# Performance work log

Measured on AMD Instinct MI355X. Metric: run time of the kernel, lower is better.

The kernel has to match this reference:

```python
import jax, jax.numpy as jnp
import numpy as np

B, S, D, H = 2, 2048, 1024, 16
DH = D // H


def setup_inputs() -> dict:
    key = jax.random.key(0)
    ks = jax.random.split(key, 12)
    std = 1.0 / np.sqrt(D)
    inp = {
        "q": jax.random.normal(ks[0], (B, S, D), jnp.float32),
        "k": jax.random.normal(ks[1], (B, S, D), jnp.float32),
        "v": jax.random.normal(ks[2], (B, S, D), jnp.float32),
        "mask": jnp.tril(jnp.ones((S, S), jnp.bool_))[None, None],  # causal [1,1,S,S]
        "wq_w": jax.random.uniform(ks[3], (D, D), jnp.float32, -std, std),
        "wq_b": jax.random.uniform(ks[4], (D,), jnp.float32, -std, std),
        "wk_w": jax.random.uniform(ks[5], (D, D), jnp.float32, -std, std),
        "wk_b": jax.random.uniform(ks[6], (D,), jnp.float32, -std, std),
        "wv_w": jax.random.uniform(ks[7], (D, D), jnp.float32, -std, std),
        "wv_b": jax.random.uniform(ks[8], (D,), jnp.float32, -std, std),
        "wo_w": jax.random.uniform(ks[9], (D, D), jnp.float32, -std, std),
        "wo_b": jax.random.uniform(ks[10], (D,), jnp.float32, -std, std),
    }
    return inp


def reference(q, k, v, mask, wq_w, wq_b, wk_w, wk_b, wv_w, wv_b, wo_w, wo_b):
    b, s, d = q.shape
    dh = d // H
    scale = jnp.sqrt(jnp.asarray(dh, q.dtype))  # scale = d_model/n_heads = d_head

    def proj(x, w, bias):
        y = x @ w.T + bias
        return y.reshape(b, -1, H, dh).transpose(0, 2, 1, 3)  # [B,H,S,dh]

    Q = proj(q, wq_w, wq_b)
    K = proj(k, wk_w, wk_b)
    V = proj(v, wv_w, wv_b)

    score = jnp.einsum("bhqd,bhkd->bhqk", Q, K) / scale
    score = jnp.where(mask, score, jnp.asarray(-1e10, score.dtype))
    attn = jax.nn.softmax(score, axis=-1)
    # dropout is identity in eval mode
    y = jnp.einsum("bhqk,bhkd->bhqd", attn, V)
    y = y.transpose(0, 2, 1, 3).reshape(b, -1, d)
    y = y @ wo_w.T + wo_b
    return y, attn
```

## Files before the change

kernel.cpp:

```cpp
#include <hip/hip_runtime.h>
#include <cstdint>

#define S_LEN   2048
#define D_MODEL 1024
#define NHEAD   16
#define DHEAD   64
#define BATCH   2
#define M_ROWS  (BATCH * S_LEN)

typedef __attribute__((ext_vector_type(8))) short bf16x8;
typedef __attribute__((ext_vector_type(4))) float f32x4;

__device__ __forceinline__ unsigned short f2bf(float f) {
    union { float f; uint32_t u; } v; v.f = f;
    uint32_t u = v.u;
    return (unsigned short)((u + 0x7FFFu + ((u >> 16) & 1u)) >> 16);
}

__device__ __forceinline__ float bf2f(uint32_t u16) {
    union { uint32_t u; float f; } x; x.u = u16 << 16; return x.f;
}

__device__ __forceinline__ uint32_t cvt_pk_bf16(float a, float b) {
    uint32_t r;
    asm("v_cvt_pk_bf16_f32 %0, %1, %2" : "=v"(r) : "v"(a), "v"(b));
    return r;
}

__device__ __forceinline__ void gload_lds16(const void* g, void* l) {
    __builtin_amdgcn_global_load_lds(
        (const __attribute__((address_space(1))) void*)g,
        (__attribute__((address_space(3))) void*)l, 16, 0, 0);
}

struct CvtArgs {
    const float* src[7];
    unsigned short* dst[7];
    int n4[7];
};
__global__ __launch_bounds__(256) void cvt_all(CvtArgs a) {
    const int which = blockIdx.y;
    const int t = blockIdx.x * 256 + threadIdx.x;
    if (t >= a.n4[which]) return;
    f32x4 v = reinterpret_cast<const f32x4*>(a.src[which])[t];
    uint2 o;
    o.x = cvt_pk_bf16(v[0], v[1]);
    o.y = cvt_pk_bf16(v[2], v[3]);
    reinterpret_cast<uint2*>(a.dst[which])[t] = o;
}

template<int MODE>
__device__ __forceinline__ void gemm_body(
    unsigned short* lA, unsigned short* lB,
    const unsigned short* __restrict__ A,
    const unsigned short* __restrict__ Bw,
    const float* __restrict__ bias,
    void* __restrict__ Cout,
    int bx, int by, float prescale)
{
    constexpr int K = 1024;
    const int tid  = threadIdx.x;
    const int lane = tid & 63;
    const int w    = tid >> 6;
    const int wr   = w >> 1, wc = w & 1;
    const int g    = lane >> 4, r16 = lane & 15;
    const int brow = by * 128;
    const int bcol = bx * 128;

    f32x4 acc[4][4];
#pragma unroll
    for (int i = 0; i < 4; ++i)
#pragma unroll
        for (int j = 0; j < 4; ++j) acc[i][j] = (f32x4){0.f, 0.f, 0.f, 0.f};

    const int rA0 = tid >> 2;
    const int cc  = (tid & 3) * 8;

    for (int kk = 0; kk < K; kk += 32) {
#pragma unroll
        for (int it = 0; it < 2; ++it) {
            int r = it * 64 + rA0;
            gload_lds16(A  + (size_t)(brow + r) * K + kk + cc, &lA[r * 32 + cc]);
            gload_lds16(Bw + (size_t)(bcol + r) * K + kk + cc, &lB[r * 32 + cc]);
        }
        __syncthreads();
        bf16x8 af[4], bfr[4];
#pragma unroll
        for (int i = 0; i < 4; ++i)
            af[i] = *reinterpret_cast<const bf16x8*>(&lA[(wr * 64 + i * 16 + r16) * 32 + g * 8]);
#pragma unroll
        for (int j = 0; j < 4; ++j)
            bfr[j] = *reinterpret_cast<const bf16x8*>(&lB[(wc * 64 + j * 16 + r16) * 32 + g * 8]);
#pragma unroll
        for (int i = 0; i < 4; ++i)
#pragma unroll
            for (int j = 0; j < 4; ++j)
                acc[i][j] = __builtin_amdgcn_mfma_f32_16x16x32_bf16(af[i], bfr[j], acc[i][j], 0, 0, 0);
        __syncthreads();
    }

#pragma unroll
    for (int i = 0; i < 4; ++i) {
#pragma unroll
        for (int j = 0; j < 4; ++j) {
            const int n = bcol + wc * 64 + j * 16 + r16;
#pragma unroll
            for (int rr = 0; rr < 4; ++rr) {
                const int m = brow + wr * 64 + i * 16 + g * 4 + rr;
                float val = acc[i][j][rr];
                if (MODE == 0) {
                    val = (val + bias[n]) * prescale;
                    int b = m >> 11, s = m & 2047;
                    int h = n >> 6,  d = n & 63;
                    ((unsigned short*)Cout)[(((size_t)(b * NHEAD + h)) * S_LEN + s) * DHEAD + d] = f2bf(val);
                } else if (MODE == 1) {
                    val += bias[m];
                    int h = m >> 6,  d = m & 63;
                    int b = n >> 11, s = n & 2047;
                    ((unsigned short*)Cout)[(((size_t)(b * NHEAD + h)) * DHEAD + d) * S_LEN + s] = f2bf(val);
                } else {
                    val += bias[n];
                    ((float*)Cout)[(size_t)m * D_MODEL + n] = val;
                }
            }
        }
    }
}

__global__ __launch_bounds__(256) void proj_all(
    const unsigned short* qb, const unsigned short* wqb, const float* wq_b, unsigned short* Qhp,
    const unsigned short* kb, const unsigned short* wkb, const float* wk_b, unsigned short* Khp,
    const unsigned short* vb, const unsigned short* wvb, const float* wv_b, unsigned short* Vtp,
    float qscale)
{
    __shared__ unsigned short lA[128 * 32];
    __shared__ unsigned short lB[128 * 32];
    const int bid = blockIdx.x;
    const int z = bid >> 8, t = bid & 255;
    if (z == 0)
        gemm_body<0>(lA, lB, qb, wqb, wq_b, Qhp, t & 7, t >> 3, qscale);
    else if (z == 1)
        gemm_body<0>(lA, lB, kb, wkb, wk_b, Khp, t & 7, t >> 3, 1.0f);
    else
        gemm_body<1>(lA, lB, wvb, vb, wv_b, Vtp, t & 31, t >> 5, 1.0f);
}

__global__ __launch_bounds__(512, 2) void attn_ctx_kernel(
    const unsigned short* __restrict__ Qh,
    const unsigned short* __restrict__ Kh,
    const unsigned short* __restrict__ Vt,
    float* __restrict__ stats,
    unsigned short* __restrict__ ctx)
{
    __shared__ unsigned short ldsK[2][64 * 64];
    __shared__ unsigned short ldsV[2][64 * 64];
    __shared__ unsigned short pS[8][16 * 72];

    const int tid  = threadIdx.x;
    const int lane = tid & 63;
    const int w    = tid >> 6;
    const int g    = lane >> 4, r16 = lane & 15;
    const int wg   = w & 3;
    const int grp  = w >> 2;

    const int lid = blockIdx.x;
    const int xcd = lid & 7;
    const int rest = lid >> 3;
    const int bh  = xcd * 4 + (rest >> 3);
    const int ii  = rest & 7;
    const int b   = bh >> 4, h = bh & 15;

    const unsigned short* Kp = Kh + (size_t)bh * S_LEN * DHEAD;
    const unsigned short* Vp = Vt + (size_t)bh * DHEAD * S_LEN;

    const int srow = tid >> 3;
    const int scol = (tid & 7) * 16;
    const int sswz = scol ^ ((srow & 7) << 4);
    const int rsw  = (r16 & 7) << 4;

    unsigned short* pl = pS[w];

    for (int pp = 0; pp < 2; ++pp) {
        const int p  = pp == 0 ? ii : 15 - ii;
        const int qh = 16 + p;
        const int ql = 15 - p;
        const int qtile = grp == 0 ? qh : ql;
        const int qw    = qtile * 64 + wg * 16;
        const int qrel  = wg * 16 + r16;
        const int myN   = qtile;

        const unsigned short* Qp = Qh + ((size_t)bh * S_LEN + qw) * DHEAD;
        bf16x8 qf[2];
#pragma unroll
        for (int d2 = 0; d2 < 2; ++d2)
            qf[d2] = *reinterpret_cast<const bf16x8*>(Qp + (size_t)r16 * DHEAD + d2 * 32 + g * 8);

        auto stageKV = [&](int kt, int buf) {
            gload_lds16((const char*)Kp + (size_t)(kt * 64 + srow) * 128 + sswz,
                        (char*)ldsK[buf] + tid * 16);
            gload_lds16((const char*)Vp + (size_t)srow * (S_LEN * 2) + (size_t)kt * 128 + sswz,
                        (char*)ldsV[buf] + tid * 16);
        };

        float l_run = 0.f;
        f32x4 of[4];
#pragma unroll
        for (int nt = 0; nt < 4; ++nt) of[nt] = (f32x4){0, 0, 0, 0};

        int buf = 0;
        stageKV(0, 0);
        __syncthreads();
        for (int t = 0; t <= qh; ++t) {
            if (t < qh) stageKV(t + 1, buf ^ 1);
            if (t <= myN) {
                const bool masked = (t == myN);
                bf16x8 kf[8];
#pragma unroll
                for (int d2 = 0; d2 < 2; ++d2)
#pragma unroll
                    for (int nt = 0; nt < 4; ++nt)
                        kf[d2 * 4 + nt] = *reinterpret_cast<const bf16x8*>(
                            (const char*)ldsK[buf] + (nt * 16 + r16) * 128 + ((d2 * 64 + g * 16) ^ rsw));
                f32x4 sf[4];
#pragma unroll
                for (int nt = 0; nt < 4; ++nt) sf[nt] = (f32x4){0, 0, 0, 0};
                __builtin_amdgcn_s_setprio(1);
#pragma unroll
                for (int d2 = 0; d2 < 2; ++d2)
#pragma unroll
                    for (int nt = 0; nt < 4; ++nt)
                        sf[nt] = __builtin_amdgcn_mfma_f32_16x16x32_bf16(kf[d2 * 4 + nt], qf[d2], sf[nt], 0, 0, 0);
                __builtin_amdgcn_s_setprio(0);
                float sum = 0.f;
#pragma unroll
                for (int nt = 0; nt < 4; ++nt)
#pragma unroll
                    for (int rr = 0; rr < 4; ++rr) {
                        float e = __builtin_amdgcn_exp2f(sf[nt][rr]);
                        if (masked && (nt * 16 + g * 4 + rr > qrel)) e = 0.f;
                        sf[nt][rr] = e;
                        sum += e;
                    }
                l_run += sum;
#pragma unroll
                for (int nt = 0; nt < 4; ++nt) {
                    uint2 pk2;
                    pk2.x = cvt_pk_bf16(sf[nt][0], sf[nt][1]);
                    pk2.y = cvt_pk_bf16(sf[nt][2], sf[nt][3]);
                    *reinterpret_cast<uint2*>(&pl[r16 * 72 + nt * 16 + g * 4]) = pk2;
                }
                __builtin_amdgcn_wave_barrier();
                __builtin_amdgcn_s_setprio(1);
#pragma unroll
                for (int kh = 0; kh < 2; ++kh) {
                    bf16x8 pa = *reinterpret_cast<const bf16x8*>(&pl[r16 * 72 + kh * 32 + g * 8]);
#pragma unroll
                    for (int nt = 0; nt < 4; ++nt) {
                        bf16x8 vf = *reinterpret_cast<const bf16x8*>(
                            (const char*)ldsV[buf] + (nt * 16 + r16) * 128 + ((kh * 64 + g * 16) ^ rsw));
                        of[nt] = __builtin_amdgcn_mfma_f32_16x16x32_bf16(vf, pa, of[nt], 0, 0, 0);
                    }
                }
                __builtin_amdgcn_s_setprio(0);
            }
            __syncthreads();
            buf ^= 1;
        }

        float lx = l_run;
        lx += __shfl_xor(lx, 16);
        lx += __shfl_xor(lx, 32);
        const float mprime = __builtin_amdgcn_logf(lx);
        if (lane < 16)
            stats[(size_t)bh * S_LEN + qw + r16] = mprime;

        const float inv = 1.f / lx;
        const size_t crow = ((size_t)b * S_LEN + qw + r16) * D_MODEL + h * DHEAD;
#pragma unroll
        for (int nt = 0; nt < 4; ++nt) {
            uint2 pk2;
            pk2.x = cvt_pk_bf16(of[nt][0] * inv, of[nt][1] * inv);
            pk2.y = cvt_pk_bf16(of[nt][2] * inv, of[nt][3] * inv);
            *reinterpret_cast<uint2*>(&ctx[crow + nt * 16 + g * 4]) = pk2;
        }
        __syncthreads();
    }
}

__global__ __launch_bounds__(256) void fused_out(
    const unsigned short* __restrict__ ctx,
    const unsigned short* __restrict__ wob,
    const float* __restrict__ wo_b,
    float* __restrict__ yout,
    const unsigned short* __restrict__ Qh,
    const unsigned short* __restrict__ Kh,
    const float* __restrict__ stats,
    float* __restrict__ attn_out)
{
    __shared__ unsigned short lds[64 * 136 + 64];
    const int bid = blockIdx.x;
    if (bid < 256) {
        gemm_body<2>(lds, lds + 128 * 32, ctx, wob, wo_b, yout, bid & 7, bid >> 3, 1.0f);
        return;
    }

    const int tid  = threadIdx.x;
    const int lane = tid & 63;
    const int w    = tid >> 6;
    const int g    = lane >> 4, r16 = lane & 15;
    const int rl   = lane >> 4;
    const int c4   = (lane & 15) * 4;

    const int pid = bid - 256;
    const int xcd = pid & 7;
    const int cid = pid >> 3;
    const int bh  = xcd * 4 + cid / 272;
    const int t   = cid % 272;
    int m = (int)((sqrtf(4.f * t + 1.f) - 1.f) * 0.5f);
    while (m * (m + 1) > t) --m;
    while ((m + 1) * (m + 2) <= t) ++m;
    int qt, c2;
    if (t < (m + 1) * (m + 1)) { qt = 2 * m;     c2 = t - m * (m + 1); }
    else                       { qt = 2 * m + 1; c2 = t - (m + 1) * (m + 1); }

    float* abase = attn_out + (size_t)bh * S_LEN * S_LEN;

    const f32x4 z4 = (f32x4){0.f, 0.f, 0.f, 0.f};
#pragma unroll
    for (int s = 0; s < 2; ++s) {
        const int tr = 2 * c2 + s;
        if (qt > tr) {
            float* dstZ = abase + (size_t)(tr * 64) * S_LEN + qt * 64;
#pragma unroll
            for (int i = 0; i < 4; ++i) {
                const int r = w * 16 + i * 4 + rl;
                __builtin_nontemporal_store(z4,
                    reinterpret_cast<f32x4*>(dstZ + (size_t)r * S_LEN + c4));
            }
        }
    }

    const int qw   = qt * 64 + w * 16;
    const int qrel = w * 16 + r16;
    const unsigned short* Qp = Qh + ((size_t)bh * S_LEN + qw) * DHEAD;
    const unsigned short* Kp = Kh + (size_t)bh * S_LEN * DHEAD;

    bf16x8 qf[2];
#pragma unroll
    for (int d2 = 0; d2 < 2; ++d2)
        qf[d2] = *reinterpret_cast<const bf16x8*>(Qp + (size_t)r16 * DHEAD + d2 * 32 + g * 8);
    const float mpr = stats[(size_t)bh * S_LEN + qw + r16];

    unsigned short* plw = lds + w * (16 * 136);

#pragma unroll
    for (int kl = 0; kl < 2; ++kl) {
        const int kt = 2 * c2 + kl;
        if (kt > qt) {
            const uint2 zz = {0u, 0u};
#pragma unroll
            for (int nt = 0; nt < 4; ++nt)
                *reinterpret_cast<uint2*>(&plw[r16 * 136 + kl * 64 + nt * 16 + g * 4]) = zz;
            continue;
        }
        bf16x8 kf[8];
#pragma unroll
        for (int d2 = 0; d2 < 2; ++d2)
#pragma unroll
            for (int nt = 0; nt < 4; ++nt)
                kf[d2 * 4 + nt] = *reinterpret_cast<const bf16x8*>(
                    Kp + (size_t)(kt * 64 + nt * 16 + r16) * DHEAD + d2 * 32 + g * 8);
        f32x4 sf[4];
#pragma unroll
        for (int nt = 0; nt < 4; ++nt) sf[nt] = (f32x4){0, 0, 0, 0};
        __builtin_amdgcn_s_setprio(1);
#pragma unroll
        for (int d2 = 0; d2 < 2; ++d2)
#pragma unroll
            for (int nt = 0; nt < 4; ++nt)
                sf[nt] = __builtin_amdgcn_mfma_f32_16x16x32_bf16(kf[d2 * 4 + nt], qf[d2], sf[nt], 0, 0, 0);
        __builtin_amdgcn_s_setprio(0);
        const bool masked = (kt == qt);
#pragma unroll
        for (int nt = 0; nt < 4; ++nt) {
#pragma unroll
            for (int rr = 0; rr < 4; ++rr) {
                float p = __builtin_amdgcn_exp2f(sf[nt][rr] - mpr);
                if (masked && (nt * 16 + g * 4 + rr > qrel)) p = 0.f;
                sf[nt][rr] = p;
            }
            uint2 pk2;
            pk2.x = cvt_pk_bf16(sf[nt][0], sf[nt][1]);
            pk2.y = cvt_pk_bf16(sf[nt][2], sf[nt][3]);
            *reinterpret_cast<uint2*>(&plw[r16 * 136 + kl * 64 + nt * 16 + g * 4]) = pk2;
        }
    }
    __builtin_amdgcn_wave_barrier();

    float* dst0 = abase + (size_t)qw * S_LEN + c2 * 128;
    const int rsub = lane >> 5;
    const int cc2  = (lane & 31) * 4;
#pragma unroll
    for (int i = 0; i < 8; ++i) {
        const int r = i * 2 + rsub;
        uint2 d = *reinterpret_cast<const uint2*>(&plw[r * 136 + cc2]);
        f32x4 o;
        o[0] = bf2f(d.x & 0xffffu);
        o[1] = bf2f(d.x >> 16);
        o[2] = bf2f(d.y & 0xffffu);
        o[3] = bf2f(d.y >> 16);
        __builtin_nontemporal_store(o, reinterpret_cast<f32x4*>(dst0 + (size_t)r * S_LEN + cc2));
    }
}

extern "C" void kernel_launch(void* const* d_in, const int* in_sizes, int n_in,
                              void* d_out, int out_size, void* d_ws, size_t ws_size,
                              hipStream_t stream)
{
    const float* q    = (const float*)d_in[0];
    const float* k    = (const float*)d_in[1];
    const float* v    = (const float*)d_in[2];
    const float* wq_w = (const float*)d_in[4];
    const float* wq_b = (const float*)d_in[5];
    const float* wk_w = (const float*)d_in[6];
    const float* wk_b = (const float*)d_in[7];
    const float* wv_w = (const float*)d_in[8];
    const float* wv_b = (const float*)d_in[9];
    const float* wo_w = (const float*)d_in[10];
    const float* wo_b = (const float*)d_in[11];

    char* ws = (char*)d_ws;
    const size_t MB = 1024 * 1024;
    unsigned short* qb  = (unsigned short*)(ws + 0 * MB);
    unsigned short* kb  = (unsigned short*)(ws + 8 * MB);
    unsigned short* vb  = (unsigned short*)(ws + 16 * MB);
    unsigned short* wqb = (unsigned short*)(ws + 24 * MB);
    unsigned short* wkb = (unsigned short*)(ws + 26 * MB);
    unsigned short* wvb = (unsigned short*)(ws + 28 * MB);
    unsigned short* wob = (unsigned short*)(ws + 30 * MB);
    unsigned short* Qhp = (unsigned short*)(ws + 32 * MB);
    unsigned short* Khp = (unsigned short*)(ws + 40 * MB);
    unsigned short* Vtp = (unsigned short*)(ws + 48 * MB);
    unsigned short* ctx = (unsigned short*)(ws + 56 * MB);
    float* stats = (float*)(ws + 0 * MB);

    float* yout = (float*)d_out;
    float* attn = yout + (size_t)M_ROWS * D_MODEL;

    CvtArgs ca;
    ca.src[0] = q;    ca.dst[0] = qb;  ca.n4[0] = M_ROWS * D_MODEL / 4;
    ca.src[1] = k;    ca.dst[1] = kb;  ca.n4[1] = M_ROWS * D_MODEL / 4;
    ca.src[2] = v;    ca.dst[2] = vb;  ca.n4[2] = M_ROWS * D_MODEL / 4;
    ca.src[3] = wq_w; ca.dst[3] = wqb; ca.n4[3] = D_MODEL * D_MODEL / 4;
    ca.src[4] = wk_w; ca.dst[4] = wkb; ca.n4[4] = D_MODEL * D_MODEL / 4;
    ca.src[5] = wv_w; ca.dst[5] = wvb; ca.n4[5] = D_MODEL * D_MODEL / 4;
    ca.src[6] = wo_w; ca.dst[6] = wob; ca.n4[6] = D_MODEL * D_MODEL / 4;
    cvt_all<<<dim3((M_ROWS * D_MODEL / 4 + 255) / 256, 7), dim3(256), 0, stream>>>(ca);

    const float qscale = 0.125f * 1.44269504088896340736f;
    proj_all<<<dim3(768), dim3(256), 0, stream>>>(
        qb, wqb, wq_b, Qhp,
        kb, wkb, wk_b, Khp,
        vb, wvb, wv_b, Vtp, qscale);

    attn_ctx_kernel<<<dim3(256), dim3(512), 0, stream>>>(Qhp, Khp, Vtp, stats, ctx);

    fused_out<<<dim3(256 + 8704), dim3(256), 0, stream>>>(
        ctx, wob, wo_b, yout, Qhp, Khp, stats, attn);
}
```

Measured before the change: 227.2 us.

## Fuse fp32-to-bf16 conversion into GEMM tile loads, drop separate convert kernel

```diff
diff --git a/kernel.cpp b/kernel.cpp
--- a/kernel.cpp
+++ b/kernel.cpp
@@ -33,27 +33,11 @@
         (__attribute__((address_space(3))) void*)l, 16, 0, 0);
 }
 
-struct CvtArgs {
-    const float* src[7];
-    unsigned short* dst[7];
-    int n4[7];
-};
-__global__ __launch_bounds__(256) void cvt_all(CvtArgs a) {
-    const int which = blockIdx.y;
-    const int t = blockIdx.x * 256 + threadIdx.x;
-    if (t >= a.n4[which]) return;
-    f32x4 v = reinterpret_cast<const f32x4*>(a.src[which])[t];
-    uint2 o;
-    o.x = cvt_pk_bf16(v[0], v[1]);
-    o.y = cvt_pk_bf16(v[2], v[3]);
-    reinterpret_cast<uint2*>(a.dst[which])[t] = o;
-}
-
-template<int MODE>
+template<int MODE, int AF32, int BF32>
 __device__ __forceinline__ void gemm_body(
     unsigned short* lA, unsigned short* lB,
-    const unsigned short* __restrict__ A,
-    const unsigned short* __restrict__ Bw,
+    const void* __restrict__ Av,
+    const void* __restrict__ Bv,
     const float* __restrict__ bias,
     void* __restrict__ Cout,
     int bx, int by, float prescale)
@@ -79,9 +63,35 @@
     for (int kk = 0; kk < K; kk += 32) {
 #pragma unroll
         for (int it = 0; it < 2; ++it) {
-            int r = it * 64 + rA0;
-            gload_lds16(A  + (size_t)(brow + r) * K + kk + cc, &lA[r * 32 + cc]);
-            gload_lds16(Bw + (size_t)(bcol + r) * K + kk + cc, &lB[r * 32 + cc]);
+            const int r = it * 64 + rA0;
+            if (AF32) {
+                const float* src = (const float*)Av + (size_t)(brow + r) * K + kk + cc;
+                float4 v0 = *reinterpret_cast<const float4*>(src);
+                float4 v1 = *reinterpret_cast<const float4*>(src + 4);
+                uint4 pk;
+                pk.x = cvt_pk_bf16(v0.x, v0.y);
+                pk.y = cvt_pk_bf16(v0.z, v0.w);
+                pk.z = cvt_pk_bf16(v1.x, v1.y);
+                pk.w = cvt_pk_bf16(v1.z, v1.w);
+                *reinterpret_cast<uint4*>(&lA[r * 32 + cc]) = pk;
+            } else {
+                gload_lds16((const unsigned short*)Av + (size_t)(brow + r) * K + kk + cc,
+                            &lA[r * 32 + cc]);
+            }
+            if (BF32) {
+                const float* src = (const float*)Bv + (size_t)(bcol + r) * K + kk + cc;
+                float4 v0 = *reinterpret_cast<const float4*>(src);
+                float4 v1 = *reinterpret_cast<const float4*>(src + 4);
+                uint4 pk;
+                pk.x = cvt_pk_bf16(v0.x, v0.y);
+                pk.y = cvt_pk_bf16(v0.z, v0.w);
+                pk.z = cvt_pk_bf16(v1.x, v1.y);
+                pk.w = cvt_pk_bf16(v1.z, v1.w);
+                *reinterpret_cast<uint4*>(&lB[r * 32 + cc]) = pk;
+            } else {
+                gload_lds16((const unsigned short*)Bv + (size_t)(bcol + r) * K + kk + cc,
+                            &lB[r * 32 + cc]);
+            }
         }
         __syncthreads();
         bf16x8 af[4], bfr[4];
@@ -128,9 +138,9 @@
 }
 
 __global__ __launch_bounds__(256) void proj_all(
-    const unsigned short* qb, const unsigned short* wqb, const float* wq_b, unsigned short* Qhp,
-    const unsigned short* kb, const unsigned short* wkb, const float* wk_b, unsigned short* Khp,
-    const unsigned short* vb, const unsigned short* wvb, const float* wv_b, unsigned short* Vtp,
+    const float* q,  const float* wq_w, const float* wq_b, unsigned short* Qhp,
+    const float* k,  const float* wk_w, const float* wk_b, unsigned short* Khp,
+    const float* v,  const float* wv_w, const float* wv_b, unsigned short* Vtp,
     float qscale)
 {
     __shared__ unsigned short lA[128 * 32];
@@ -138,11 +148,11 @@
     const int bid = blockIdx.x;
     const int z = bid >> 8, t = bid & 255;
     if (z == 0)
-        gemm_body<0>(lA, lB, qb, wqb, wq_b, Qhp, t & 7, t >> 3, qscale);
+        gemm_body<0, 1, 1>(lA, lB, q, wq_w, wq_b, Qhp, t & 7, t >> 3, qscale);
     else if (z == 1)
-        gemm_body<0>(lA, lB, kb, wkb, wk_b, Khp, t & 7, t >> 3, 1.0f);
+        gemm_body<0, 1, 1>(lA, lB, k, wk_w, wk_b, Khp, t & 7, t >> 3, 1.0f);
     else
-        gemm_body<1>(lA, lB, wvb, vb, wv_b, Vtp, t & 31, t >> 5, 1.0f);
+        gemm_body<1, 1, 1>(lA, lB, wv_w, v, wv_b, Vtp, t & 31, t >> 5, 1.0f);
 }
 
 __global__ __launch_bounds__(512, 2) void attn_ctx_kernel(
@@ -289,7 +299,7 @@
 
 __global__ __launch_bounds__(256) void fused_out(
     const unsigned short* __restrict__ ctx,
-    const unsigned short* __restrict__ wob,
+    const float* __restrict__ wo_w,
     const float* __restrict__ wo_b,
     float* __restrict__ yout,
     const unsigned short* __restrict__ Qh,
@@ -300,7 +310,7 @@
     __shared__ unsigned short lds[64 * 136 + 64];
     const int bid = blockIdx.x;
     if (bid < 256) {
-        gemm_body<2>(lds, lds + 128 * 32, ctx, wob, wo_b, yout, bid & 7, bid >> 3, 1.0f);
+        gemm_body<2, 0, 1>(lds, lds + 128 * 32, ctx, wo_w, wo_b, yout, bid & 7, bid >> 3, 1.0f);
         return;
     }
 
@@ -431,13 +441,6 @@
 
     char* ws = (char*)d_ws;
     const size_t MB = 1024 * 1024;
-    unsigned short* qb  = (unsigned short*)(ws + 0 * MB);
-    unsigned short* kb  = (unsigned short*)(ws + 8 * MB);
-    unsigned short* vb  = (unsigned short*)(ws + 16 * MB);
-    unsigned short* wqb = (unsigned short*)(ws + 24 * MB);
-    unsigned short* wkb = (unsigned short*)(ws + 26 * MB);
-    unsigned short* wvb = (unsigned short*)(ws + 28 * MB);
-    unsigned short* wob = (unsigned short*)(ws + 30 * MB);
     unsigned short* Qhp = (unsigned short*)(ws + 32 * MB);
     unsigned short* Khp = (unsigned short*)(ws + 40 * MB);
     unsigned short* Vtp = (unsigned short*)(ws + 48 * MB);
@@ -447,24 +450,14 @@
     float* yout = (float*)d_out;
     float* attn = yout + (size_t)M_ROWS * D_MODEL;
 
-    CvtArgs ca;
-    ca.src[0] = q;    ca.dst[0] = qb;  ca.n4[0] = M_ROWS * D_MODEL / 4;
-    ca.src[1] = k;    ca.dst[1] = kb;  ca.n4[1] = M_ROWS * D_MODEL / 4;
-    ca.src[2] = v;    ca.dst[2] = vb;  ca.n4[2] = M_ROWS * D_MODEL / 4;
-    ca.src[3] = wq_w; ca.dst[3] = wqb; ca.n4[3] = D_MODEL * D_MODEL / 4;
-    ca.src[4] = wk_w; ca.dst[4] = wkb; ca.n4[4] = D_MODEL * D_MODEL / 4;
-    ca.src[5] = wv_w; ca.dst[5] = wvb; ca.n4[5] = D_MODEL * D_MODEL / 4;
-    ca.src[6] = wo_w; ca.dst[6] = wob; ca.n4[6] = D_MODEL * D_MODEL / 4;
-    cvt_all<<<dim3((M_ROWS * D_MODEL / 4 + 255) / 256, 7), dim3(256), 0, stream>>>(ca);
-
     const float qscale = 0.125f * 1.44269504088896340736f;
     proj_all<<<dim3(768), dim3(256), 0, stream>>>(
-        qb, wqb, wq_b, Qhp,
-        kb, wkb, wk_b, Khp,
-        vb, wvb, wv_b, Vtp, qscale);
+        q, wq_w, wq_b, Qhp,
+        k, wk_w, wk_b, Khp,
+        v, wv_w, wv_b, Vtp, qscale);
 
     attn_ctx_kernel<<<dim3(256), dim3(512), 0, stream>>>(Qhp, Khp, Vtp, stats, ctx);
 
     fused_out<<<dim3(256 + 8704), dim3(256), 0, stream>>>(
-        ctx, wob, wo_b, yout, Qhp, Khp, stats, attn);
-}
+        ctx, wo_w, wo_b, yout, Qhp, Khp, stats, attn);
+}
```

Result: slower. 232.3 us (+2.2%).
